# Kernel tuning notes

Measured on AMD Instinct MI355X. Metric: run time of the kernel, lower is better.

Reference implementation:

```python
import jax, jax.numpy as jnp
import numpy as np

B, SQ, SKV, H, NH = 2, 2048, 2048, 1024, 16
HD = H // NH  # head dim = 64


def setup_inputs() -> dict:
    key = jax.random.key(0)
    ks = jax.random.split(key, 10)
    s = 1.0 / np.sqrt(H)
    return {
        "query_states": jax.random.normal(ks[0], (B, SQ, H), jnp.float32),
        "key_value_states": jax.random.normal(ks[1], (B, SKV, H), jnp.float32),
        "attention_mask": jnp.ones((B, SQ, SKV), jnp.float32),
        "Wq": jax.random.normal(ks[2], (H, H), jnp.float32) * s,
        "bq": jnp.zeros((H,), jnp.float32),
        "Wk": jax.random.normal(ks[3], (H, H), jnp.float32) * s,
        "Wv": jax.random.normal(ks[4], (H, H), jnp.float32) * s,
        "bv": jnp.zeros((H,), jnp.float32),
        "Wo": jax.random.normal(ks[5], (H, H), jnp.float32) * s,
        "bo": jnp.zeros((H,), jnp.float32),
    }


def reference(query_states, key_value_states, attention_mask, Wq, bq, Wk, Wv, bv, Wo, bo):
    # projections (torch Linear: x @ W.T + b; key proj has NO bias)
    q = query_states @ Wq.T + bq            # [B,SQ,H]
    k = key_value_states @ Wk.T              # [B,SKV,H]
    v = key_value_states @ Wv.T + bv         # [B,SKV,H]
    # split heads -> [B, NH, S, HD]
    q = q.reshape(B, SQ, NH, HD).transpose(0, 2, 1, 3)
    k = k.reshape(B, SKV, NH, HD).transpose(0, 2, 1, 3)
    v = v.reshape(B, SKV, NH, HD).transpose(0, 2, 1, 3)
    scale = 1.0 / np.sqrt(HD)
    scores = jnp.einsum("bhqd,bhkd->bhqk", q * scale, k)
    # additive mask: (1 - mask) * -10000, broadcast over heads
    scores = scores + ((1.0 - attention_mask) * -10000.0)[:, None, :, :]
    probs = jax.nn.softmax(scores, axis=-1)  # dropout p=0 (eval) -> identity
    ctx = jnp.einsum("bhqk,bhkd->bhqd", probs, v)
    ctx = ctx.transpose(0, 2, 1, 3).reshape(B, SQ, H)
    return ctx @ Wo.T + bo
```

## Files before the change

kernel.cpp:

```cpp
#include <hip/hip_runtime.h>

typedef unsigned short u16;
typedef unsigned int u32;
typedef short s16x8 __attribute__((ext_vector_type(8)));
typedef float f32x4 __attribute__((ext_vector_type(4)));

#define AS1 __attribute__((address_space(1)))
#define AS3 __attribute__((address_space(3)))

#define LOG2E 1.4426950408889634f

__device__ __forceinline__ u16 f2bf(float f) {
  unsigned u = __float_as_uint(f);
  u += 0x7fffu + ((u >> 16) & 1u);
  return (u16)(u >> 16);
}
__device__ __forceinline__ float bf2f(u16 b) {
  return __uint_as_float(((unsigned)b) << 16);
}
__device__ __forceinline__ u32 cvtpk(float lo, float hi) {
  u32 r;
  asm("v_cvt_pk_bf16_f32 %0, %1, %2" : "=v"(r) : "v"(lo), "v"(hi));
  return r;
}
__device__ __forceinline__ void gld16(const void* g, void* l) {
  __builtin_amdgcn_global_load_lds((const AS1 unsigned int*)g,
                                   (AS3 unsigned int*)l, 16, 0, 0);
}

__global__ __launch_bounds__(256) void prep_kernel(
    const float* __restrict__ qs, const float* __restrict__ kvs, const float* __restrict__ mk,
    const float* __restrict__ wq, const float* __restrict__ wk, const float* __restrict__ wv,
    const float* __restrict__ wo,
    u16* __restrict__ q_bf, u16* __restrict__ kv_bf, u16* __restrict__ am_bf,
    u16* __restrict__ wq_bf, u16* __restrict__ wk_bf, u16* __restrict__ wv_bf,
    u16* __restrict__ wo_bf)
{
  const int stride = gridDim.x * blockDim.x;
  const float mscale = -10000.f * LOG2E;
  for (int v = blockIdx.x * blockDim.x + threadIdx.x; v < 5242880; v += stride) {
    const float* s; u16* d; int off; bool ismask = false;
    if (v < 1048576)      { s = qs;  d = q_bf;  off = v; }
    else if (v < 2097152) { s = kvs; d = kv_bf; off = v - 1048576; }
    else if (v < 2359296) { s = wq;  d = wq_bf; off = v - 2097152; }
    else if (v < 2621440) { s = wk;  d = wk_bf; off = v - 2359296; }
    else if (v < 2883584) { s = wv;  d = wv_bf; off = v - 2621440; }
    else if (v < 3145728) { s = wo;  d = wo_bf; off = v - 2883584; }
    else                  { s = mk;  d = am_bf; off = v - 3145728; ismask = true; }
    float4 f = ((const float4*)s)[off];
    if (ismask) {
      f.x = (1.f - f.x) * mscale; f.y = (1.f - f.y) * mscale;
      f.z = (1.f - f.z) * mscale; f.w = (1.f - f.w) * mscale;
    }
    uint2 o;
    o.x = cvtpk(f.x, f.y);
    o.y = cvtpk(f.z, f.w);
    ((uint2*)d)[off] = o;
  }
}

__global__ __launch_bounds__(256) void flag_kernel(const u16* __restrict__ am,
                                                   u32* __restrict__ flags)
{
  const int fid = blockIdx.x;
  const int kt = fid & 31, qt = (fid >> 5) & 15, b = fid >> 9;
  const int t = threadIdx.x;
  const int row = t >> 1, half = t & 1;
  const u16* p = am + ((size_t)(b * 2048 + qt * 128 + row)) * 2048 + kt * 64 + half * 32;
  const uint4 v0 = *(const uint4*)p;
  const uint4 v1 = *(const uint4*)(p + 16);
  const u32 acc = v0.x | v0.y | v0.z | v0.w | v1.x | v1.y | v1.z | v1.w;
  const bool z = (acc & 0x7fff7fffu) == 0;
  const bool wz = __all(z);
  __shared__ int ok[4];
  if ((t & 63) == 0) ok[t >> 6] = wz;
  __syncthreads();
  if (t == 0 && ok[0] && ok[1] && ok[2] && ok[3])
    atomicOr(&flags[(b << 4) + qt], 1u << kt);
}

template<int EPI>
__device__ __forceinline__ void gemm_body(
    const u16* __restrict__ A, const u16* __restrict__ W, const float* __restrict__ bias,
    void* __restrict__ outp, float alpha, int m0, int n0)
{
  __shared__ u16 As[3][4096], Bs[3][4096];
  const int tid = threadIdx.x, wave = tid >> 6, lane = tid & 63;
  const int l15 = lane & 15, l4 = lane >> 4;
  const int wr = wave >> 1, wc = wave & 1;

  const int srow = wave * 16 + (lane >> 2);
  const int sslot = ((lane & 3) ^ ((lane >> 3) & 3)) * 8;
  const u16* aS0 = A + (size_t)(m0 + srow) * 1024 + sslot;
  const u16* aS1 = A + (size_t)(m0 + 64 + srow) * 1024 + sslot;
  const u16* bS0 = W + (size_t)(n0 + srow) * 1024 + sslot;
  const u16* bS1 = W + (size_t)(n0 + 64 + srow) * 1024 + sslot;
  const int dOff0 = wave * 512, dOff1 = 2048 + wave * 512;

  const int fswz = ((l15 >> 1) & 3);
  const int afBase = (wr * 64 + l15) * 32 + ((l4 ^ fswz) * 8);
  const int bfBase = (wc * 64 + l15) * 32 + ((l4 ^ fswz) * 8);

  f32x4 acc[4][4] = {};

  auto stage = [&](int buf, int kt) {
    const int ko = kt * 32;
    gld16(aS0 + ko, &As[buf][dOff0]);
    gld16(aS1 + ko, &As[buf][dOff1]);
    gld16(bS0 + ko, &Bs[buf][dOff0]);
    gld16(bS1 + ko, &Bs[buf][dOff1]);
  };

  stage(0, 0);
  stage(1, 1);

  int cb = 0;
  for (int kt = 0; kt < 32; ++kt) {
    if (kt < 31) asm volatile("s_waitcnt vmcnt(4)" ::: "memory");
    else         asm volatile("s_waitcnt vmcnt(0)" ::: "memory");
    __builtin_amdgcn_s_barrier();
    asm volatile("" ::: "memory");
    if (kt < 30) {
      int sb = cb + 2; if (sb >= 3) sb -= 3;
      stage(sb, kt + 2);
    }
    s16x8 af[4], bf[4];
    #pragma unroll
    for (int m = 0; m < 4; ++m) af[m] = *(const s16x8*)&As[cb][afBase + m * 512];
    #pragma unroll
    for (int n = 0; n < 4; ++n) bf[n] = *(const s16x8*)&Bs[cb][bfBase + n * 512];
    #pragma unroll
    for (int m = 0; m < 4; ++m)
      #pragma unroll
      for (int n = 0; n < 4; ++n)
        acc[m][n] = __builtin_amdgcn_mfma_f32_16x16x32_bf16(af[m], bf[n], acc[m][n], 0, 0, 0);
    asm volatile("" ::: "memory");
    cb = (cb + 1 == 3) ? 0 : cb + 1;
  }

  #pragma unroll
  for (int n = 0; n < 4; ++n) {
    const int col = n0 + wc * 64 + n * 16 + l15;
    #pragma unroll
    for (int m = 0; m < 4; ++m) {
      #pragma unroll
      for (int r = 0; r < 4; ++r) {
        const int row = m0 + wr * 64 + m * 16 + l4 * 4 + r;
        if constexpr (EPI == 0) {
          const float val = (acc[m][n][r] + (bias ? bias[col] : 0.f)) * alpha;
          const int bb = row >> 11, ss = row & 2047, hh = col >> 6, dd = col & 63;
          ((u16*)outp)[(((size_t)(bb * 16 + hh)) * 2048 + ss) * 64 + dd] = f2bf(val);
        } else if constexpr (EPI == 1) {
          ((float*)outp)[(size_t)row * 1024 + col] = acc[m][n][r] + (bias ? bias[col] : 0.f);
        } else {
          const float val = acc[m][n][r] + bias[row];
          const int hh = row >> 6, dd = row & 63, bb = col >> 11, ss = col & 2047;
          ((u16*)outp)[(((size_t)(bb * 16 + hh)) * 64 + dd) * 2048 + ss] = f2bf(val);
        }
      }
    }
  }
}

__global__ __launch_bounds__(256) void gemm_nt0(
    const u16* __restrict__ A, const u16* __restrict__ W, const float* __restrict__ bias,
    u16* __restrict__ out, float alpha)
{
  const int bid = blockIdx.x;
  const int swz = (bid & 7) * 32 + (bid >> 3);
  gemm_body<0>(A, W, bias, out, alpha, (swz >> 3) * 128, (swz & 7) * 128);
}

__global__ __launch_bounds__(256) void gemm_vT(
    const u16* __restrict__ wvb, const u16* __restrict__ kvbf, const float* __restrict__ bv,
    u16* __restrict__ Vt)
{
  const int bid = blockIdx.x;
  const int m0 = (bid >> 5) * 128;
  const int n0 = ((bid & 7) + ((bid >> 3) & 3) * 8) * 128;
  gemm_body<2>(wvb, kvbf, bv, Vt, 1.0f, m0, n0);
}

__global__ __launch_bounds__(256) void gemm_fin(
    const u16* __restrict__ ctx, const u16* __restrict__ wob,
    const float* __restrict__ bo, float* __restrict__ out)
{
  const int bid = blockIdx.x;
  const int swz = (bid & 7) * 32 + (bid >> 3);
  gemm_body<1>(ctx, wob, bo, out, 1.0f, (swz >> 3) * 128, (swz & 7) * 128);
}

__global__ __launch_bounds__(256) void attn_kernel(
    const u16* __restrict__ Qh, const u16* __restrict__ Kh,
    const u16* __restrict__ Vt, const u16* __restrict__ am,
    const u32* __restrict__ fbitsp, u16* __restrict__ ctx)
{
  __shared__ u16 Ks[2][4096];
  __shared__ u16 Vs[2][4096];
  __shared__ u16 Pl[4][2][1024];
  const int tid = threadIdx.x, wave = tid >> 6, lane = tid & 63;
  const int l15 = lane & 15, l4 = lane >> 4;
  const int x7 = l15 & 7;
  const int bid = blockIdx.x;
  const int pos = (bid & 7) * 64 + (bid >> 3);
  const int hh = pos >> 4, qt = pos & 15;
  const int b = hh >> 4, h = hh & 15;
  const int q0 = qt * 128;
  const u16* Qb = Qh + (size_t)hh * 2048 * 64;
  const u16* Kb = Kh + (size_t)hh * 2048 * 64;
  const u16* Vb = Vt + (size_t)hh * 64 * 2048;
  const u32 fbits = fbitsp[(b << 4) + qt];

  s16x8 qf[2][2];
  const u16* amrow[2];
  #pragma unroll
  for (int g = 0; g < 2; ++g) {
    const int qrow = q0 + wave * 32 + g * 16 + l15;
    qf[g][0] = *(const s16x8*)(Qb + (size_t)qrow * 64 + l4 * 8);
    qf[g][1] = *(const s16x8*)(Qb + (size_t)qrow * 64 + 32 + l4 * 8);
    amrow[g] = am + ((size_t)b * 2048 + qrow) * 2048;
  }

  const int sr = wave * 16 + (lane >> 3);
  const int ss = ((lane & 7) ^ ((lane >> 3) & 7)) * 8;
  const u16* kS0 = Kb + (size_t)sr * 64 + ss;
  const u16* kS1 = Kb + (size_t)(sr + 8) * 64 + ss;
  const u16* vS0 = Vb + (size_t)sr * 2048 + ss;
  const u16* vS1 = Vb + (size_t)(sr + 8) * 2048 + ss;
  const int kd0 = wave * 1024, kd1 = kd0 + 512;

  auto stage = [&](int buf, int kt) {
    const int kv0 = kt * 64;
    gld16(kS0 + (size_t)kv0 * 64, &Ks[buf][kd0]);
    gld16(kS1 + (size_t)kv0 * 64, &Ks[buf][kd1]);
    gld16(vS0 + kv0, &Vs[buf][kd0]);
    gld16(vS1 + kv0, &Vs[buf][kd1]);
  };

  f32x4 of[2][4] = {};
  float m_run[2] = {-1e30f, -1e30f}, l_run[2] = {0.f, 0.f};

  stage(0, 0);
  asm volatile("s_waitcnt vmcnt(0)" ::: "memory");
  __builtin_amdgcn_s_barrier();
  asm volatile("" ::: "memory");

  int cur = 0;
  for (int kt = 0; kt < 32; ++kt) {
    if (kt < 31) stage(cur ^ 1, kt + 1);
    const int kv0 = kt * 64;
    const bool skip = (fbits >> kt) & 1u;

    ushort4 mk4[2][4];
    if (!skip) {
      #pragma unroll
      for (int g = 0; g < 2; ++g)
        #pragma unroll
        for (int nf = 0; nf < 4; ++nf)
          mk4[g][nf] = *(const ushort4*)(amrow[g] + kv0 + nf * 16 + l4 * 4);
    }

    f32x4 sf[2][4];
    __builtin_amdgcn_s_setprio(1);
    #pragma unroll
    for (int nf = 0; nf < 4; ++nf) {
      const s16x8 ka0 = *(const s16x8*)&Ks[cur][nf * 1024 + l15 * 64 + ((l4 ^ x7) * 8)];
      const s16x8 ka1 = *(const s16x8*)&Ks[cur][nf * 1024 + l15 * 64 + (((4 + l4) ^ x7) * 8)];
      #pragma unroll
      for (int g = 0; g < 2; ++g) {
        f32x4 s = {0.f, 0.f, 0.f, 0.f};
        s = __builtin_amdgcn_mfma_f32_16x16x32_bf16(ka0, qf[g][0], s, 0, 0, 0);
        s = __builtin_amdgcn_mfma_f32_16x16x32_bf16(ka1, qf[g][1], s, 0, 0, 0);
        sf[g][nf] = s;
      }
    }
    __builtin_amdgcn_s_setprio(0);

    #pragma unroll
    for (int g = 0; g < 2; ++g) {
      float tmax = -1e30f;
      #pragma unroll
      for (int nf = 0; nf < 4; ++nf)
        #pragma unroll
        for (int r = 0; r < 4; ++r) {
          float sv = sf[g][nf][r];
          if (!skip) sv += bf2f(((const u16*)&mk4[g][nf])[r]);
          sf[g][nf][r] = sv;
          tmax = fmaxf(tmax, sv);
        }
      tmax = fmaxf(tmax, __shfl_xor(tmax, 16));
      tmax = fmaxf(tmax, __shfl_xor(tmax, 32));

      const float mOld = m_run[g];
      float mn = mOld;
      if (!__all(tmax <= mOld + 11.54f)) {
        mn = fmaxf(mOld, tmax);
        const float sc = exp2f(mOld - mn);
        m_run[g] = mn;
        l_run[g] *= sc;
        float sq[4];
        #pragma unroll
        for (int r = 0; r < 4; ++r) sq[r] = __shfl(sc, l4 * 4 + r);
        #pragma unroll
        for (int nd = 0; nd < 4; ++nd)
          #pragma unroll
          for (int r = 0; r < 4; ++r) of[g][nd][r] *= sq[r];
      }

      float psum = 0.f;
      u32* pw = (u32*)&Pl[wave][g][0];
      #pragma unroll
      for (int nf = 0; nf < 4; ++nf) {
        const float p0 = exp2f(sf[g][nf][0] - mn), p1 = exp2f(sf[g][nf][1] - mn);
        const float p2 = exp2f(sf[g][nf][2] - mn), p3 = exp2f(sf[g][nf][3] - mn);
        psum += (p0 + p1) + (p2 + p3);
        u32* w = pw + l15 * 32 + (((nf * 2 + (l4 >> 1)) ^ x7) * 4) + (l4 & 1) * 2;
        w[0] = cvtpk(p0, p1);
        w[1] = cvtpk(p2, p3);
      }
      psum += __shfl_xor(psum, 16);
      psum += __shfl_xor(psum, 32);
      l_run[g] += psum;
    }

    __builtin_amdgcn_s_setprio(1);
    #pragma unroll
    for (int kh = 0; kh < 2; ++kh) {
      s16x8 pa[2];
      #pragma unroll
      for (int g = 0; g < 2; ++g)
        pa[g] = *(const s16x8*)&Pl[wave][g][l15 * 64 + (((kh * 4 + l4) ^ x7) * 8)];
      #pragma unroll
      for (int nd = 0; nd < 4; ++nd) {
        const s16x8 vb = *(const s16x8*)&Vs[cur][nd * 1024 + l15 * 64 + (((kh * 4 + l4) ^ x7) * 8)];
        #pragma unroll
        for (int g = 0; g < 2; ++g)
          of[g][nd] = __builtin_amdgcn_mfma_f32_16x16x32_bf16(pa[g], vb, of[g][nd], 0, 0, 0);
      }
    }
    __builtin_amdgcn_s_setprio(0);

    if (kt < 31) {
      asm volatile("s_waitcnt vmcnt(0)" ::: "memory");
      __builtin_amdgcn_s_barrier();
      asm volatile("" ::: "memory");
    }
    cur ^= 1;
  }

  #pragma unroll
  for (int g = 0; g < 2; ++g) {
    const float inv = 1.f / l_run[g];
    float invq[4];
    #pragma unroll
    for (int r = 0; r < 4; ++r) invq[r] = __shfl(inv, l4 * 4 + r);
    #pragma unroll
    for (int r = 0; r < 4; ++r) {
      const int qg = q0 + wave * 32 + g * 16 + l4 * 4 + r;
      const size_t rowbase = ((size_t)b * 2048 + qg) * 1024 + h * 64;
      #pragma unroll
      for (int nd = 0; nd < 4; ++nd)
        ctx[rowbase + nd * 16 + l15] = f2bf(of[g][nd][r] * invq[r]);
    }
  }
}

extern "C" void kernel_launch(void* const* d_in, const int* in_sizes, int n_in,
                              void* d_out, int out_size, void* d_ws, size_t ws_size,
                              hipStream_t stream)
{
  const float* qs = (const float*)d_in[0];
  const float* kvs = (const float*)d_in[1];
  const float* mk = (const float*)d_in[2];
  const float* Wq = (const float*)d_in[3];
  const float* bq = (const float*)d_in[4];
  const float* Wk = (const float*)d_in[5];
  const float* Wv = (const float*)d_in[6];
  const float* bv = (const float*)d_in[7];
  const float* Wo = (const float*)d_in[8];
  const float* bo = (const float*)d_in[9];
  float* out = (float*)d_out;

  char* ws = (char*)d_ws;
  u16* q_bf  = (u16*)(ws + 0);
  u16* kv_bf = (u16*)(ws + 8388608);
  u16* wq_bf = (u16*)(ws + 16777216);
  u16* wk_bf = (u16*)(ws + 18874368);
  u16* wv_bf = (u16*)(ws + 20971520);
  u16* wo_bf = (u16*)(ws + 23068672);
  u16* am_bf = (u16*)(ws + 25165824);
  u16* Qhp   = (u16*)(ws + 41943040);
  u16* Khp   = (u16*)(ws + 50331648);
  u16* Vtp   = (u16*)(ws + 58720256);
  u16* ctxp  = (u16*)(ws + 67108864);
  u32* flagsp = (u32*)wq_bf;

  prep_kernel<<<dim3(2048), dim3(256), 0, stream>>>(
      qs, kvs, mk, Wq, Wk, Wv, Wo, q_bf, kv_bf, am_bf, wq_bf, wk_bf, wv_bf, wo_bf);

  gemm_nt0<<<dim3(256), dim3(256), 0, stream>>>(q_bf, wq_bf, bq, Qhp, 0.125f * LOG2E);
  gemm_nt0<<<dim3(256), dim3(256), 0, stream>>>(kv_bf, wk_bf, nullptr, Khp, 1.0f);
  gemm_vT <<<dim3(256), dim3(256), 0, stream>>>(wv_bf, kv_bf, bv, Vtp);

  hipMemsetAsync(flagsp, 0, 128, stream);
  flag_kernel<<<dim3(1024), dim3(256), 0, stream>>>(am_bf, flagsp);

  attn_kernel<<<dim3(512), dim3(256), 0, stream>>>(Qhp, Khp, Vtp, am_bf, flagsp, ctxp);

  gemm_fin<<<dim3(256), dim3(256), 0, stream>>>(ctxp, wo_bf, bo, out);
}
```

Measured before the change: 348.1 us.

## Merge QKV GEMMs into one 512-thread launch and compute softmax row sums via MFMA

The three projection GEMMs become a single launch using a 2D grid. Each block now runs 8 waves, and each wave owns a 32x64 sub-tile instead of 64x64, which halves accumulator registers and raises parallelism per block. The mask-flag kernel writes one byte per tile instead of using atomics, so the memset is no longer needed; the attention kernel packs those bytes into a bitmask. Inside attention, the softmax denominator is accumulated with an extra MFMA against a ones vector instead of per-row adds and cross-lane shuffles, trading extra matrix-core work for fewer VALU operations and shuffles.

```diff
diff --git a/kernel.cpp b/kernel.cpp
--- a/kernel.cpp
+++ b/kernel.cpp
@@ -1,6 +1,7 @@
 #include <hip/hip_runtime.h>
 
 typedef unsigned short u16;
+typedef unsigned char u8;
 typedef unsigned int u32;
 typedef short s16x8 __attribute__((ext_vector_type(8)));
 typedef float f32x4 __attribute__((ext_vector_type(4)));
@@ -60,7 +61,7 @@
 }
 
 __global__ __launch_bounds__(256) void flag_kernel(const u16* __restrict__ am,
-                                                   u32* __restrict__ flags)
+                                                   u8* __restrict__ flags)
 {
   const int fid = blockIdx.x;
   const int kt = fid & 31, qt = (fid >> 5) & 15, b = fid >> 9;
@@ -75,8 +76,7 @@
   __shared__ int ok[4];
   if ((t & 63) == 0) ok[t >> 6] = wz;
   __syncthreads();
-  if (t == 0 && ok[0] && ok[1] && ok[2] && ok[3])
-    atomicOr(&flags[(b << 4) + qt], 1u << kt);
+  if (t == 0) flags[fid] = (ok[0] & ok[1] & ok[2] & ok[3]) ? 1 : 0;
 }
 
 template<int EPI>
@@ -90,25 +90,21 @@
   const int wr = wave >> 1, wc = wave & 1;
 
   const int srow = wave * 16 + (lane >> 2);
-  const int sslot = ((lane & 3) ^ ((lane >> 3) & 3)) * 8;
-  const u16* aS0 = A + (size_t)(m0 + srow) * 1024 + sslot;
-  const u16* aS1 = A + (size_t)(m0 + 64 + srow) * 1024 + sslot;
-  const u16* bS0 = W + (size_t)(n0 + srow) * 1024 + sslot;
-  const u16* bS1 = W + (size_t)(n0 + 64 + srow) * 1024 + sslot;
-  const int dOff0 = wave * 512, dOff1 = 2048 + wave * 512;
-
-  const int fswz = ((l15 >> 1) & 3);
-  const int afBase = (wr * 64 + l15) * 32 + ((l4 ^ fswz) * 8);
+  const int soct = ((lane & 3) ^ ((lane >> 3) & 3)) * 8;
+  const u16* aS = A + (size_t)(m0 + srow) * 1024 + soct;
+  const u16* bS = W + (size_t)(n0 + srow) * 1024 + soct;
+  const int dOff = wave * 512;
+
+  const int fswz = (l15 >> 1) & 3;
+  const int afBase = (wr * 32 + l15) * 32 + ((l4 ^ fswz) * 8);
   const int bfBase = (wc * 64 + l15) * 32 + ((l4 ^ fswz) * 8);
 
-  f32x4 acc[4][4] = {};
+  f32x4 acc[2][4] = {};
 
   auto stage = [&](int buf, int kt) {
     const int ko = kt * 32;
-    gld16(aS0 + ko, &As[buf][dOff0]);
-    gld16(aS1 + ko, &As[buf][dOff1]);
-    gld16(bS0 + ko, &Bs[buf][dOff0]);
-    gld16(bS1 + ko, &Bs[buf][dOff1]);
+    gld16(aS + ko, &As[buf][dOff]);
+    gld16(bS + ko, &Bs[buf][dOff]);
   };
 
   stage(0, 0);
@@ -116,7 +112,7 @@
 
   int cb = 0;
   for (int kt = 0; kt < 32; ++kt) {
-    if (kt < 31) asm volatile("s_waitcnt vmcnt(4)" ::: "memory");
+    if (kt < 31) asm volatile("s_waitcnt vmcnt(2)" ::: "memory");
     else         asm volatile("s_waitcnt vmcnt(0)" ::: "memory");
     __builtin_amdgcn_s_barrier();
     asm volatile("" ::: "memory");
@@ -124,13 +120,13 @@
       int sb = cb + 2; if (sb >= 3) sb -= 3;
       stage(sb, kt + 2);
     }
-    s16x8 af[4], bf[4];
-    #pragma unroll
-    for (int m = 0; m < 4; ++m) af[m] = *(const s16x8*)&As[cb][afBase + m * 512];
+    s16x8 af[2], bf[4];
+    #pragma unroll
+    for (int m = 0; m < 2; ++m) af[m] = *(const s16x8*)&As[cb][afBase + m * 512];
     #pragma unroll
     for (int n = 0; n < 4; ++n) bf[n] = *(const s16x8*)&Bs[cb][bfBase + n * 512];
     #pragma unroll
-    for (int m = 0; m < 4; ++m)
+    for (int m = 0; m < 2; ++m)
       #pragma unroll
       for (int n = 0; n < 4; ++n)
         acc[m][n] = __builtin_amdgcn_mfma_f32_16x16x32_bf16(af[m], bf[n], acc[m][n], 0, 0, 0);
@@ -142,10 +138,10 @@
   for (int n = 0; n < 4; ++n) {
     const int col = n0 + wc * 64 + n * 16 + l15;
     #pragma unroll
-    for (int m = 0; m < 4; ++m) {
+    for (int m = 0; m < 2; ++m) {
       #pragma unroll
       for (int r = 0; r < 4; ++r) {
-        const int row = m0 + wr * 64 + m * 16 + l4 * 4 + r;
+        const int row = m0 + wr * 32 + m * 16 + l4 * 4 + r;
         if constexpr (EPI == 0) {
           const float val = (acc[m][n][r] + (bias ? bias[col] : 0.f)) * alpha;
           const int bb = row >> 11, ss = row & 2047, hh = col >> 6, dd = col & 63;
@@ -162,26 +158,25 @@
   }
 }
 
-__global__ __launch_bounds__(256) void gemm_nt0(
-    const u16* __restrict__ A, const u16* __restrict__ W, const float* __restrict__ bias,
-    u16* __restrict__ out, float alpha)
+__global__ __launch_bounds__(512) void gemm_qkv(
+    const u16* __restrict__ qbf, const u16* __restrict__ kvbf,
+    const u16* __restrict__ wqb, const u16* __restrict__ wkb, const u16* __restrict__ wvb,
+    const float* __restrict__ bq, const float* __restrict__ bv,
+    u16* __restrict__ Qh, u16* __restrict__ Kh, u16* __restrict__ Vt)
 {
   const int bid = blockIdx.x;
   const int swz = (bid & 7) * 32 + (bid >> 3);
-  gemm_body<0>(A, W, bias, out, alpha, (swz >> 3) * 128, (swz & 7) * 128);
-}
-
-__global__ __launch_bounds__(256) void gemm_vT(
-    const u16* __restrict__ wvb, const u16* __restrict__ kvbf, const float* __restrict__ bv,
-    u16* __restrict__ Vt)
-{
-  const int bid = blockIdx.x;
-  const int m0 = (bid >> 5) * 128;
-  const int n0 = ((bid & 7) + ((bid >> 3) & 3) * 8) * 128;
-  gemm_body<2>(wvb, kvbf, bv, Vt, 1.0f, m0, n0);
-}
-
-__global__ __launch_bounds__(256) void gemm_fin(
+  const int which = blockIdx.y;
+  if (which == 0)
+    gemm_body<0>(qbf, wqb, bq, Qh, 0.125f * LOG2E, (swz >> 3) * 128, (swz & 7) * 128);
+  else if (which == 1)
+    gemm_body<0>(kvbf, wkb, nullptr, Kh, 1.0f, (swz >> 3) * 128, (swz & 7) * 128);
+  else
+    gemm_body<2>(wvb, kvbf, bv, Vt, 1.0f, (bid >> 5) * 128,
+                 ((bid & 7) + ((bid >> 3) & 3) * 8) * 128);
+}
+
+__global__ __launch_bounds__(512) void gemm_fin(
     const u16* __restrict__ ctx, const u16* __restrict__ wob,
     const float* __restrict__ bo, float* __restrict__ out)
 {
@@ -193,7 +188,7 @@
 __global__ __launch_bounds__(256) void attn_kernel(
     const u16* __restrict__ Qh, const u16* __restrict__ Kh,
     const u16* __restrict__ Vt, const u16* __restrict__ am,
-    const u32* __restrict__ fbitsp, u16* __restrict__ ctx)
+    const u8* __restrict__ flags, u16* __restrict__ ctx)
 {
   __shared__ u16 Ks[2][4096];
   __shared__ u16 Vs[2][4096];
@@ -209,7 +204,13 @@
   const u16* Qb = Qh + (size_t)hh * 2048 * 64;
   const u16* Kb = Kh + (size_t)hh * 2048 * 64;
   const u16* Vb = Vt + (size_t)hh * 64 * 2048;
-  const u32 fbits = fbitsp[(b << 4) + qt];
+
+  u32 fbits = 0;
+  {
+    const u8* fb = flags + (b * 16 + qt) * 32;
+    #pragma unroll
+    for (int i = 0; i < 32; ++i) fbits |= (fb[i] ? 1u : 0u) << i;
+  }
 
   s16x8 qf[2][2];
   const u16* amrow[2];
@@ -221,6 +222,8 @@
     amrow[g] = am + ((size_t)b * 2048 + qrow) * 2048;
   }
 
+  const s16x8 ones = {16256, 16256, 16256, 16256, 16256, 16256, 16256, 16256};
+
   const int sr = wave * 16 + (lane >> 3);
   const int ss = ((lane & 7) ^ ((lane >> 3) & 7)) * 8;
   const u16* kS0 = Kb + (size_t)sr * 64 + ss;
@@ -238,7 +241,8 @@
   };
 
   f32x4 of[2][4] = {};
-  float m_run[2] = {-1e30f, -1e30f}, l_run[2] = {0.f, 0.f};
+  f32x4 lr[2] = {};
+  float m_run[2] = {-1e30f, -1e30f};
 
   stage(0, 0);
   asm volatile("s_waitcnt vmcnt(0)" ::: "memory");
@@ -297,30 +301,26 @@
         mn = fmaxf(mOld, tmax);
         const float sc = exp2f(mOld - mn);
         m_run[g] = mn;
-        l_run[g] *= sc;
         float sq[4];
         #pragma unroll
         for (int r = 0; r < 4; ++r) sq[r] = __shfl(sc, l4 * 4 + r);
+        #pragma unroll
+        for (int r = 0; r < 4; ++r) lr[g][r] *= sq[r];
         #pragma unroll
         for (int nd = 0; nd < 4; ++nd)
           #pragma unroll
           for (int r = 0; r < 4; ++r) of[g][nd][r] *= sq[r];
       }
 
-      float psum = 0.f;
       u32* pw = (u32*)&Pl[wave][g][0];
       #pragma unroll
       for (int nf = 0; nf < 4; ++nf) {
         const float p0 = exp2f(sf[g][nf][0] - mn), p1 = exp2f(sf[g][nf][1] - mn);
         const float p2 = exp2f(sf[g][nf][2] - mn), p3 = exp2f(sf[g][nf][3] - mn);
-        psum += (p0 + p1) + (p2 + p3);
         u32* w = pw + l15 * 32 + (((nf * 2 + (l4 >> 1)) ^ x7) * 4) + (l4 & 1) * 2;
         w[0] = cvtpk(p0, p1);
         w[1] = cvtpk(p2, p3);
       }
-      psum += __shfl_xor(psum, 16);
-      psum += __shfl_xor(psum, 32);
-      l_run[g] += psum;
     }
 
     __builtin_amdgcn_s_setprio(1);
@@ -337,6 +337,9 @@
         for (int g = 0; g < 2; ++g)
           of[g][nd] = __builtin_amdgcn_mfma_f32_16x16x32_bf16(pa[g], vb, of[g][nd], 0, 0, 0);
       }
+      #pragma unroll
+      for (int g = 0; g < 2; ++g)
+        lr[g] = __builtin_amdgcn_mfma_f32_16x16x32_bf16(pa[g], ones, lr[g], 0, 0, 0);
     }
     __builtin_amdgcn_s_setprio(0);
 
@@ -350,17 +353,14 @@
 
   #pragma unroll
   for (int g = 0; g < 2; ++g) {
-    const float inv = 1.f / l_run[g];
-    float invq[4];
-    #pragma unroll
-    for (int r = 0; r < 4; ++r) invq[r] = __shfl(inv, l4 * 4 + r);
     #pragma unroll
     for (int r = 0; r < 4; ++r) {
+      const float invq = 1.f / lr[g][r];
       const int qg = q0 + wave * 32 + g * 16 + l4 * 4 + r;
       const size_t rowbase = ((size_t)b * 2048 + qg) * 1024 + h * 64;
       #pragma unroll
       for (int nd = 0; nd < 4; ++nd)
-        ctx[rowbase + nd * 16 + l15] = f2bf(of[g][nd][r] * invq[r]);
+        ctx[rowbase + nd * 16 + l15] = f2bf(of[g][nd][r] * invq);
     }
   }
 }
@@ -393,19 +393,17 @@
   u16* Khp   = (u16*)(ws + 50331648);
   u16* Vtp   = (u16*)(ws + 58720256);
   u16* ctxp  = (u16*)(ws + 67108864);
-  u32* flagsp = (u32*)wq_bf;
+  u8* flagsp = (u8*)wq_bf;
 
   prep_kernel<<<dim3(2048), dim3(256), 0, stream>>>(
       qs, kvs, mk, Wq, Wk, Wv, Wo, q_bf, kv_bf, am_bf, wq_bf, wk_bf, wv_bf, wo_bf);
 
-  gemm_nt0<<<dim3(256), dim3(256), 0, stream>>>(q_bf, wq_bf, bq, Qhp, 0.125f * LOG2E);
-  gemm_nt0<<<dim3(256), dim3(256), 0, stream>>>(kv_bf, wk_bf, nullptr, Khp, 1.0f);
-  gemm_vT <<<dim3(256), dim3(256), 0, stream>>>(wv_bf, kv_bf, bv, Vtp);
-
-  hipMemsetAsync(flagsp, 0, 128, stream);
+  gemm_qkv<<<dim3(256, 3), dim3(512), 0, stream>>>(
+      q_bf, kv_bf, wq_bf, wk_bf, wv_bf, bq, bv, Qhp, Khp, Vtp);
+
   flag_kernel<<<dim3(1024), dim3(256), 0, stream>>>(am_bf, flagsp);
 
   attn_kernel<<<dim3(512), dim3(256), 0, stream>>>(Qhp, Khp, Vtp, am_bf, flagsp, ctxp);
 
-  gemm_fin<<<dim3(256), dim3(256), 0, stream>>>(ctxp, wo_bf, bo, out);
-}
+  gemm_fin<<<dim3(256), dim3(512), 0, stream>>>(ctxp, wo_bf, bo, out);
+}
```

Result: faster. 284.3 us (-18.3%).
